# Kernel optimization log

Measured on AMD Instinct MI355X. Metric: run time of the kernel, lower is better.

The kernel has to match this reference:

```python
import math
import jax, jax.numpy as jnp
import numpy as np

B, S, D, H, L, V = 2, 1024, 1024, 16, 6, 256
HD = D // H  # 64
PAD = 0


def setup_inputs() -> dict:
    key = jax.random.key(0)
    ks = jax.random.split(key, 22)
    s = 0.02
    f32 = jnp.float32
    inp = {
        "x": jax.random.randint(ks[0], (B, S), 0, V, dtype=jnp.int32),
        "emb": (jax.random.normal(ks[1], (V, D)) * s).astype(f32),
        "Wq": (jax.random.normal(ks[2], (L, D, D)) * s).astype(f32),
        "bq": jnp.zeros((L, D), f32),
        "Wk": (jax.random.normal(ks[3], (L, D, D)) * s).astype(f32),
        "bk": jnp.zeros((L, D), f32),
        "Wv": (jax.random.normal(ks[4], (L, D, D)) * s).astype(f32),
        "bv": jnp.zeros((L, D), f32),
        "Wo": (jax.random.normal(ks[5], (L, D, D)) * s).astype(f32),
        "bo": jnp.zeros((L, D), f32),
        "W1": (jax.random.normal(ks[6], (L, D, D // 2)) * s).astype(f32),
        "b1": jnp.zeros((L, D // 2), f32),
        "W2": (jax.random.normal(ks[7], (L, D // 2, D)) * s).astype(f32),
        "b2": jnp.zeros((L, D), f32),
        "g1": jnp.ones((L, D), f32),
        "be1": jnp.zeros((L, D), f32),
        "g2": jnp.ones((L, D), f32),
        "be2": jnp.zeros((L, D), f32),
        "E": jax.random.normal(ks[8], (L, S, HD)).astype(f32),  # relative pos embeddings, non-trainable
        "Wf": (jax.random.normal(ks[9], (D, V)) * s).astype(f32),
        "bf": jnp.zeros((V,), f32),
    }
    return inp


def _layernorm(x, g, b, eps=1e-6):
    mu = jnp.mean(x, axis=-1, keepdims=True)
    var = jnp.mean((x - mu) ** 2, axis=-1, keepdims=True)
    return (x - mu) * jax.lax.rsqrt(var + eps) * g + b


def _pos_encoding():
    # embed[p, i] = sin(p * exp(-ln(1e4)*i/D) * exp(ln(1e4)*(i%2)/D) + 0.5*pi*(i%2))
    i = jnp.arange(D, dtype=jnp.float32)
    par = jnp.mod(i, 2.0)
    rate = jnp.exp(-math.log(10000.0) * i / D) * jnp.exp(math.log(10000.0) * par / D)
    pos = jnp.arange(S, dtype=jnp.float32)
    return jnp.sin(pos[:, None] * rate[None, :] + 0.5 * math.pi * par[None, :])  # [S, D]


def _skew(QE):
    # Music Transformer skewing: pad one col on the left, reshape, drop first row.
    padded = jnp.pad(QE, ((0, 0), (0, 0), (0, 0), (1, 0)))  # [B,H,S,S+1]
    reshaped = padded.reshape(B, H, S + 1, S)
    return reshaped[:, :, 1:, :]  # [B,H,S,S]


def reference(x, emb, Wq, bq, Wk, bk, Wv, bv, Wo, bo, W1, b1, W2, b2,
              g1, be1, g2, be2, E, Wf, bf):
    pe = _pos_encoding()
    # look-ahead mask: pad positions OR strictly-future positions
    pad_mask = (x == PAD)[:, None, None, :]                      # [B,1,1,S]
    causal = jnp.triu(jnp.ones((S, S), bool), k=1)[None, None]   # [1,1,S,S]
    neg = (pad_mask | causal).astype(jnp.float32) * -1e9         # [B,1,S,S]
    # QE mask: keep qe[i, j] only where j >= S-1-i (upper-right triangle)
    idx = jnp.arange(S)
    qe_mask = (idx[None, :] >= (S - 1 - idx)[:, None]).astype(jnp.float32)

    h = emb[x] * math.sqrt(D) + pe[None]  # [B,S,D]
    scale = 1.0 / math.sqrt(HD)
    for l in range(L):
        q = (h @ Wq[l] + bq[l]).reshape(B, S, H, HD).transpose(0, 2, 1, 3)
        k = (h @ Wk[l] + bk[l]).reshape(B, S, H, HD).transpose(0, 2, 1, 3)
        v = (h @ Wv[l] + bv[l]).reshape(B, S, H, HD).transpose(0, 2, 1, 3)
        QE = jnp.einsum('bhld,md->bhlm', q, E[l]) * qe_mask
        Srel = _skew(QE)
        logits = (jnp.einsum('bhld,bhmd->bhlm', q, k) + Srel) * scale + neg
        aw = jax.nn.softmax(logits, axis=-1)
        attn = jnp.einsum('bhlm,bhmd->bhld', aw, v)
        attn = attn.transpose(0, 2, 1, 3).reshape(B, S, D)
        ao = attn @ Wo[l] + bo[l]
        o1 = _layernorm(ao, g1[l], be1[l])          # NOTE: no residual, as in source
        f = jax.nn.relu(o1 @ W1[l] + b1[l]) @ W2[l] + b2[l]
        h = _layernorm(f, g2[l], be2[l])
    return h @ Wf + bf  # [B,S,V]
```

## Files before the change

### kernel.cpp

```cpp
#include <hip/hip_runtime.h>
#include <hip/hip_bf16.h>


typedef __attribute__((ext_vector_type(8))) short  s8_t;
typedef __attribute__((ext_vector_type(4))) short  s4_t;
typedef __attribute__((ext_vector_type(8))) __bf16 bf8_t;
typedef __attribute__((ext_vector_type(4))) float  f4v;

static __device__ __forceinline__ short f2bf(float f) {
  union { float f; unsigned u; } a; a.f = f;
  unsigned u = a.u;
  u += 0x7fffu + ((u >> 16) & 1u);
  return (short)(u >> 16);
}
static __device__ __forceinline__ float bf2f(short s) {
  union { float f; unsigned u; } a;
  a.u = ((unsigned)(unsigned short)s) << 16;
  return a.f;
}
static __device__ __forceinline__ f4v mfma16(s8_t a, s8_t b, f4v c) {
  return __builtin_amdgcn_mfma_f32_16x16x32_bf16(
      __builtin_bit_cast(bf8_t, a), __builtin_bit_cast(bf8_t, b), c, 0, 0, 0);
}
static __device__ __forceinline__ void gld16(const short* g, short* l) {
  __builtin_amdgcn_global_load_lds(
      (const __attribute__((address_space(1))) void*)g,
      (__attribute__((address_space(3))) void*)l, 16, 0, 0);
}

static __device__ const int IT_TAB[40] = {
  15,15,15,15, 14,14,14,14, 13,13,13,13, 12,12,12,12,
  11,11,11, 10,10,10, 9,9,9, 8,8,8,
  7,7, 6,6, 5,5, 4,4, 3, 2, 1, 0};
static __device__ const int CW_TAB[40] = {
  0,1,2,3, 0,1,2,3, 0,1,2,3, 0,1,2,3,
  0,1,2, 0,1,2, 0,1,2, 0,1,2,
  0,1, 0,1, 0,1, 0,1, 0, 0, 0, 0};

__global__ __launch_bounds__(256) void prep_weights(
    const float* __restrict__ Wq, const float* __restrict__ Wk,
    const float* __restrict__ Wv, const float* __restrict__ Wo,
    const float* __restrict__ W1, const float* __restrict__ W2,
    const float* __restrict__ Wf,
    short* __restrict__ qkvT, short* __restrict__ WoT, short* __restrict__ W1T,
    short* __restrict__ W2T, short* __restrict__ WfT) {
  __shared__ float tile[64][69];
  int z = blockIdx.x;
  const float* in; short* out; int R, C; long outBS; int rowOff = 0;
  if (z < 4608) {
    R = 1024; C = 1024; outBS = (long)3072 * 1024; out = qkvT;
    if (z < 1536)      { in = Wq; }
    else if (z < 3072) { in = Wk; rowOff = 1024; z -= 1536; }
    else               { in = Wv; rowOff = 2048; z -= 3072; }
  } else if (z < 6144) { in = Wo; out = WoT; R = 1024; C = 1024; outBS = (long)1024 * 1024; z -= 4608; }
  else if (z < 6912)   { in = W1; out = W1T; R = 1024; C = 512;  outBS = (long)512 * 1024;  z -= 6144; }
  else if (z < 7680)   { in = W2; out = W2T; R = 512;  C = 1024; outBS = (long)1024 * 512;  z -= 6912; }
  else                 { in = Wf; out = WfT; R = 1024; C = 256;  outBS = 0;                 z -= 7680; }
  const int nx = C >> 6, ny = R >> 6;
  const int per = nx * ny;
  const int l = z / per, rem = z % per;
  const int cx = rem % nx, cy = rem / nx;
  in += (long)l * R * C;
  out += (long)l * outBS + (long)rowOff * R;
  const int c0 = cx * 64, r0 = cy * 64;
  const int tid = threadIdx.x;

  const int lr = tid >> 4, lc4 = tid & 15;
#pragma unroll
  for (int p = 0; p < 4; p++) {
    const int row = p * 16 + lr;
    const float4 v = *(const float4*)(in + (long)(r0 + row) * C + c0 + lc4 * 4);
    tile[row][lc4 * 4 + 0] = v.x;
    tile[row][lc4 * 4 + 1] = v.y;
    tile[row][lc4 * 4 + 2] = v.z;
    tile[row][lc4 * 4 + 3] = v.w;
  }
  __syncthreads();
  const int seg = tid & 7;
#pragma unroll
  for (int q = 0; q < 2; q++) {
    const int oc = q * 32 + (tid >> 3);
    s8_t o;
#pragma unroll
    for (int j = 0; j < 8; j++) o[j] = f2bf(tile[seg * 8 + j][oc]);
    *(s8_t*)(out + (long)(c0 + oc) * R + r0 + seg * 8) = o;
  }
}

__global__ __launch_bounds__(256) void prep_misc(
    const int* __restrict__ x, const float* __restrict__ emb,
    const float* __restrict__ E,
    const float* __restrict__ bq, const float* __restrict__ bk,
    const float* __restrict__ bv,
    short* __restrict__ h, short* __restrict__ Ebf,
    float* __restrict__ qkvB, int* __restrict__ fnp) {
  const int z = blockIdx.x;
  const int tid = threadIdx.x;
  if (z < 2048) {
    const int s = z & 1023;
    const int xv = x[z];
    const int c = tid << 2;
    const float4 e = *(const float4*)(emb + (long)xv * 1024 + c);
    const float ev[4] = {e.x, e.y, e.z, e.w};
    s4_t o;
#pragma unroll
    for (int i = 0; i < 4; i++) {
      const int d = c + i;
      const float par = (float)(d & 1);
      const float rate = expf(-9.210340371976184f * (float)d / 1024.0f) *
                         expf(9.210340371976184f * par / 1024.0f);
      const float pe = sinf((float)s * rate + 1.5707963267948966f * par);
      o[i] = f2bf(ev[i] * 32.0f + pe);
    }
    *(s4_t*)(h + (long)z * 1024 + c) = o;
  } else if (z < 2432) {
    const long i = ((long)(z - 2048) * 256 + tid) * 4;
    const float4 t = *(const float4*)(E + i);
    s4_t o = {f2bf(t.x), f2bf(t.y), f2bf(t.z), f2bf(t.w)};
    *(s4_t*)(Ebf + i) = o;
  } else if (z < 2504) {
    const int idx = (z - 2432) * 256 + tid;
    const int l = idx / 3072, n = idx % 3072;
    float v = (n < 1024) ? bq[l * 1024 + n]
            : (n < 2048) ? bk[l * 1024 + n - 1024]
                         : bv[l * 1024 + n - 2048];
    qkvB[idx] = v;
  } else {
    if (tid < 64) {
      const int b = z - 2504;
      int first = 1024;
      for (int j0 = 0; j0 < 1024; j0 += 64) {
        unsigned long long m = __ballot(x[b * 1024 + j0 + tid] != 0);
        if (m) { first = j0 + __ffsll(m) - 1; break; }
      }
      if (tid == 0) fnp[b] = first;
    }
  }
}

__global__ __launch_bounds__(256) void ln_kernel(const short* __restrict__ in,
                                                 short* __restrict__ out,
                                                 const float* __restrict__ g,
                                                 const float* __restrict__ be) {
  __shared__ float red[4];
  __shared__ float red2[4];
  const int row = blockIdx.x;
  const int tid = threadIdx.x;
  const int c = tid << 2;
  const s4_t xv = *(const s4_t*)(in + (long)row * 1024 + c);
  const float x0 = bf2f(xv[0]), x1 = bf2f(xv[1]), x2 = bf2f(xv[2]), x3 = bf2f(xv[3]);
  float s = x0 + x1 + x2 + x3;
#pragma unroll
  for (int off = 1; off < 64; off <<= 1) s += __shfl_xor(s, off);
  const int wave = tid >> 6, lane = tid & 63;
  if (lane == 0) red[wave] = s;
  __syncthreads();
  const float mu = (red[0] + red[1] + red[2] + red[3]) * (1.0f / 1024.0f);
  const float d0 = x0 - mu, d1 = x1 - mu, d2 = x2 - mu, d3 = x3 - mu;
  float q = d0 * d0 + d1 * d1 + d2 * d2 + d3 * d3;
#pragma unroll
  for (int off = 1; off < 64; off <<= 1) q += __shfl_xor(q, off);
  if (lane == 0) red2[wave] = q;
  __syncthreads();
  const float var = (red2[0] + red2[1] + red2[2] + red2[3]) * (1.0f / 1024.0f);
  const float rs = rsqrtf(var + 1e-6f);
  const float4 gv = *(const float4*)(g + c);
  const float4 bv = *(const float4*)(be + c);
  s4_t o = {f2bf(d0 * rs * gv.x + bv.x), f2bf(d1 * rs * gv.y + bv.y),
            f2bf(d2 * rs * gv.z + bv.z), f2bf(d3 * rs * gv.w + bv.w)};
  *(s4_t*)(out + (long)row * 1024 + c) = o;
}

template <int BM, int BN, int WR, int WC, int OUT_BF16, int RELU>
__global__ __launch_bounds__(256) void gemm_lds(
    const short* __restrict__ A, const short* __restrict__ BT,
    void* __restrict__ Cv, const float* __restrict__ biasp,
    int K, int lda, int ldb, int ldc) {
  constexpr int AR = BM / 64, BR = BN / 64;
  constexpr int FI = BM / WR / 16, FJ = BN / WC / 16;
  __shared__ short As[BM * 32];
  __shared__ short Bs[BN * 32];
  const int bm = blockIdx.y * BM, bn = blockIdx.x * BN;
  const int tid = threadIdx.x;
  const int wave = tid >> 6, lane = tid & 63;
  const int quad = lane >> 4, l16 = lane & 15;
  const int wr = wave / WC, wc = wave % WC;
  const int wm = wr * (BM / WR), wn = wc * (BN / WC);

  const short* Ag = A + (long)(bm + wave * 16 + (lane >> 2)) * lda + ((lane & 3) << 3);
  const short* Bg = BT + (long)(bn + wave * 16 + (lane >> 2)) * ldb + ((lane & 3) << 3);

  f4v acc[FI][FJ];
#pragma unroll
  for (int i = 0; i < FI; i++)
#pragma unroll
    for (int j = 0; j < FJ; j++) {
      f4v zz = {0.f, 0.f, 0.f, 0.f};
      acc[i][j] = zz;
    }

  for (int k0 = 0; k0 < K; k0 += 32) {
#pragma unroll
    for (int r = 0; r < AR; r++)
      gld16(Ag + (long)r * 64 * lda + k0, As + r * 2048 + wave * 512);
#pragma unroll
    for (int r = 0; r < BR; r++)
      gld16(Bg + (long)r * 64 * ldb + k0, Bs + r * 2048 + wave * 512);
    __syncthreads();
    s8_t af[FI], bfr[FJ];
#pragma unroll
    for (int t = 0; t < FI; t++)
      af[t] = *(const s8_t*)&As[(wm + t * 16 + l16) * 32 + quad * 8];
#pragma unroll
    for (int t = 0; t < FJ; t++)
      bfr[t] = *(const s8_t*)&Bs[(wn + t * 16 + l16) * 32 + quad * 8];
#pragma unroll
    for (int ti = 0; ti < FI; ti++)
#pragma unroll
      for (int tj = 0; tj < FJ; tj++)
        acc[ti][tj] = mfma16(af[ti], bfr[tj], acc[ti][tj]);
    __syncthreads();
  }

#pragma unroll
  for (int ti = 0; ti < FI; ti++) {
#pragma unroll
    for (int tj = 0; tj < FJ; tj++) {
      const int n = bn + wn + tj * 16 + l16;
      const float bval = biasp ? biasp[n] : 0.f;
#pragma unroll
      for (int r = 0; r < 4; r++) {
        const int m = bm + wm + ti * 16 + quad * 4 + r;
        float vv = acc[ti][tj][r] + bval;
        if (RELU) vv = fmaxf(vv, 0.f);
        if (OUT_BF16) ((short*)Cv)[(long)m * ldc + n] = f2bf(vv);
        else          ((float*)Cv)[(long)m * ldc + n] = vv;
      }
    }
  }
}

__global__ __launch_bounds__(256) void attn_main(
    const short* __restrict__ qkv, const short* __restrict__ Eb,
    const int* __restrict__ xids, const int* __restrict__ fnp,
    float* __restrict__ PO, float* __restrict__ PM, float* __restrict__ PL,
    short* __restrict__ outb) {
  __shared__ short Ks2[2][8][64][8];
  __shared__ short Vt[64][72];
  __shared__ short Gs[4][16][88];
  __shared__ short knegs[1024];

  const int bh = blockIdx.x, b = bh >> 4, hh = bh & 15;
  const int yy = blockIdx.y;
  const bool fbp = (yy >= 40);
  const int itile = fbp ? (yy - 40) : IT_TAB[yy];
  const int cw = fbp ? 0 : CW_TAB[yy];
  const int fb = fnp[b];
  const int i0g = itile * 64;
  if (fbp && fb <= i0g) return;

  const int tid = threadIdx.x;
  const int wave = tid >> 6, lane = tid & 63, quad = lane >> 4, l16 = lane & 15;
  const int i0 = i0g + wave * 16;

  {
    const short neg = f2bf(-1e9f);
#pragma unroll
    for (int t = 0; t < 4; t++) {
      const int idx = t * 256 + tid;
      knegs[idx] = (xids[b * 1024 + idx] == 0) ? neg : (short)0;
    }
  }

  s8_t aq[2];
  {
    const short* qp = qkv + ((long)(b * 1024 + i0 + l16)) * 3072 + hh * 64 + quad * 8;
    aq[0] = *(const s8_t*)qp;
    aq[1] = *(const s8_t*)(qp + 32);
  }

  f4v o[4];
#pragma unroll
  for (int nt = 0; nt < 4; nt++) { f4v zz = {0.f, 0.f, 0.f, 0.f}; o[nt] = zz; }
  float m_run[4] = {-INFINITY, -INFINITY, -INFINITY, -INFINITY};
  float l_run[4] = {0.f, 0.f, 0.f, 0.f};

  const short* kbase = qkv + (long)b * 1024 * 3072 + 1024 + hh * 64 + wave * 8;
  const short* vbase = qkv + (long)b * 1024 * 3072 + 2048 + hh * 64 + wave * 16;
  short* gs = &Gs[wave][0][0];

  const int jBeg = fbp ? 0 : cw * 256;
  const int jEnd = fbp ? 1024 : min(cw * 256 + 256, i0g + 64);

  s8_t vr0, vr1;
  {
    const long k1 = min(jBeg + lane, 1023);
    gld16(kbase + k1 * 3072, &Ks2[0][wave][0][0]);
    gld16(kbase + k1 * 3072 + 32, &Ks2[0][wave + 4][0][0]);
    const short* vrow = vbase + k1 * 3072;
    vr0 = *(const s8_t*)(vrow);
    vr1 = *(const s8_t*)(vrow + 8);
#pragma unroll
    for (int t = 0; t < 8; t++) {
      Vt[wave * 16 + t][lane] = vr0[t];
      Vt[wave * 16 + 8 + t][lane] = vr1[t];
    }
  }

  int pb = 0;
  for (int j0 = jBeg; j0 < jEnd; j0 += 64) {
    const bool hasNext = (j0 + 64 < jEnd);
    __syncthreads();

    {
      const int mW = 1008 - i0g - wave * 16 + j0;
#pragma unroll
      for (int t = 0; t < 5; t++) {
        const int m = min(mW + t * 16 + l16, 1023);
        const short* ep = Eb + m * 64 + quad * 8;
        const s8_t eb0 = *(const s8_t*)ep;
        const s8_t eb1 = *(const s8_t*)(ep + 32);
        f4v g = {0.f, 0.f, 0.f, 0.f};
        g = mfma16(aq[0], eb0, g);
        g = mfma16(aq[1], eb1, g);
#pragma unroll
        for (int r = 0; r < 4; r++)
          gs[(quad * 4 + r) * 88 + t * 16 + l16] = f2bf(g[r]);
      }
    }

    if (hasNext) {
      const long k1 = min(j0 + 64 + lane, 1023);
      gld16(kbase + k1 * 3072, &Ks2[pb ^ 1][wave][0][0]);
      gld16(kbase + k1 * 3072 + 32, &Ks2[pb ^ 1][wave + 4][0][0]);
      const short* vrow = vbase + k1 * 3072;
      vr0 = *(const s8_t*)(vrow);
      vr1 = *(const s8_t*)(vrow + 8);
    }

    float p[4][4];
    const int irow = i0 + quad * 4;
#pragma unroll
    for (int jt = 0; jt < 4; jt++) {
      const s8_t k0f = *(const s8_t*)&Ks2[pb][quad][jt * 16 + l16][0];
      const s8_t k1f = *(const s8_t*)&Ks2[pb][4 + quad][jt * 16 + l16][0];
      f4v zz = {0.f, 0.f, 0.f, 0.f};
      zz = mfma16(aq[0], k0f, zz);
      zz = mfma16(aq[1], k1f, zz);
      const int j = j0 + jt * 16 + l16;
      const float kn = bf2f(knegs[j]);
#pragma unroll
      for (int r = 0; r < 4; r++) {
        const int rr = quad * 4 + r;
        const float smv = bf2f(gs[rr * 87 + 15 + jt * 16 + l16]);
        const bool causal = (j <= irow + r);
        const float srel = causal ? smv : 0.f;
        const float kk = fbp ? 0.f : (causal ? kn : -1e9f);
        p[jt][r] = (zz[r] + srel) * 0.125f + kk;
      }
    }

    float alpha[4];
#pragma unroll
    for (int r = 0; r < 4; r++) {
      float mx = p[0][r];
#pragma unroll
      for (int jt = 1; jt < 4; jt++) mx = fmaxf(mx, p[jt][r]);
      mx = fmaxf(mx, __shfl_xor(mx, 1));
      mx = fmaxf(mx, __shfl_xor(mx, 2));
      mx = fmaxf(mx, __shfl_xor(mx, 4));
      mx = fmaxf(mx, __shfl_xor(mx, 8));
      const float mnew = fmaxf(m_run[r], mx);
      alpha[r] = __expf(m_run[r] - mnew);
      float ps = 0.f;
#pragma unroll
      for (int jt = 0; jt < 4; jt++) {
        p[jt][r] = __expf(p[jt][r] - mnew);
        ps += p[jt][r];
      }
      ps += __shfl_xor(ps, 1);
      ps += __shfl_xor(ps, 2);
      ps += __shfl_xor(ps, 4);
      ps += __shfl_xor(ps, 8);
      l_run[r] = l_run[r] * alpha[r] + ps;
      m_run[r] = mnew;
    }

#pragma unroll
    for (int jt = 0; jt < 4; jt++)
#pragma unroll
      for (int r = 0; r < 4; r++)
        gs[(quad * 4 + r) * 88 + jt * 16 + l16] = f2bf(p[jt][r]);
#pragma unroll
    for (int nt = 0; nt < 4; nt++)
#pragma unroll
      for (int r = 0; r < 4; r++)
        o[nt][r] *= alpha[r];

#pragma unroll
    for (int ks4 = 0; ks4 < 2; ks4++) {
      const s8_t ap = *(const s8_t*)&gs[l16 * 88 + ks4 * 32 + quad * 8];
#pragma unroll
      for (int nt = 0; nt < 4; nt++) {
        const s8_t vf = *(const s8_t*)&Vt[nt * 16 + l16][ks4 * 32 + quad * 8];
        o[nt] = mfma16(ap, vf, o[nt]);
      }
    }

    __syncthreads();
    if (hasNext) {
#pragma unroll
      for (int t = 0; t < 8; t++) {
        Vt[wave * 16 + t][lane] = vr0[t];
        Vt[wave * 16 + 8 + t][lane] = vr1[t];
      }
    }
    pb ^= 1;
  }

  if (fbp) {
#pragma unroll
    for (int nt = 0; nt < 4; nt++)
#pragma unroll
      for (int r = 0; r < 4; r++) {
        const int i = i0 + quad * 4 + r;
        if (i < fb)
          outb[((long)(b * 1024 + i)) * 1024 + hh * 64 + nt * 16 + l16] =
              f2bf(o[nt][r] / l_run[r]);
      }
  } else if (yy >= 36) {
#pragma unroll
    for (int nt = 0; nt < 4; nt++)
#pragma unroll
      for (int r = 0; r < 4; r++) {
        const int i = i0 + quad * 4 + r;
        if (i >= fb)
          outb[((long)(b * 1024 + i)) * 1024 + hh * 64 + nt * 16 + l16] =
              f2bf(o[nt][r] / l_run[r]);
      }
  } else {
    const long part = (long)(bh * 16 + itile) * 4 + cw;
    float* po = PO + part * 4096;
#pragma unroll
    for (int nt = 0; nt < 4; nt++)
#pragma unroll
      for (int r = 0; r < 4; r++) {
        const int row = wave * 16 + quad * 4 + r;
        po[row * 64 + nt * 16 + l16] = o[nt][r];
      }
    if (l16 == 0) {
#pragma unroll
      for (int r = 0; r < 4; r++) {
        const int row = wave * 16 + quad * 4 + r;
        PM[part * 64 + row] = m_run[r];
        PL[part * 64 + row] = l_run[r];
      }
    }
  }
}

__global__ __launch_bounds__(256) void attn_combine(
    const float* __restrict__ PO, const float* __restrict__ PM,
    const float* __restrict__ PL, const int* __restrict__ fnp,
    short* __restrict__ outb) {
  const int id = blockIdx.x;
  const int bh = id / 12, itile = 4 + id % 12;
  const int b = bh >> 4, hh = bh & 15;
  const int nc = (itile >> 2) + 1;
  const int row = threadIdx.x >> 2, seg = (threadIdx.x & 3) << 4;
  const long base = (long)(bh * 16 + itile) * 4;
  const int i = itile * 64 + row;
  if (i < fnp[b]) return;

  float mv[4];
  float M = -INFINITY;
  for (int c = 0; c < nc; c++) {
    mv[c] = PM[(base + c) * 64 + row];
    M = fmaxf(M, mv[c]);
  }
  f4v acc[4];
#pragma unroll
  for (int t = 0; t < 4; t++) { f4v zz = {0.f, 0.f, 0.f, 0.f}; acc[t] = zz; }
  float l = 0.f;
  for (int c = 0; c < nc; c++) {
    const float w = __expf(mv[c] - M);
    l += w * PL[(base + c) * 64 + row];
    const float* po = PO + (base + c) * 4096 + row * 64 + seg;
#pragma unroll
    for (int t = 0; t < 4; t++) {
      const f4v v = *(const f4v*)(po + t * 4);
      acc[t] += w * v;
    }
  }
  const float inv = 1.0f / l;
  short* op = outb + ((long)(b * 1024 + i)) * 1024 + hh * 64 + seg;
#pragma unroll
  for (int t = 0; t < 4; t++) {
    s4_t o = {f2bf(acc[t][0] * inv), f2bf(acc[t][1] * inv),
              f2bf(acc[t][2] * inv), f2bf(acc[t][3] * inv)};
    *(s4_t*)(op + t * 4) = o;
  }
}

extern "C" void kernel_launch(void* const* d_in, const int* in_sizes, int n_in,
                              void* d_out, int out_size, void* d_ws, size_t ws_size,
                              hipStream_t stream) {
  const int*   x   = (const int*)d_in[0];
  const float* emb = (const float*)d_in[1];
  const float* Wq  = (const float*)d_in[2];
  const float* bq  = (const float*)d_in[3];
  const float* Wk  = (const float*)d_in[4];
  const float* bk  = (const float*)d_in[5];
  const float* Wv  = (const float*)d_in[6];
  const float* bv  = (const float*)d_in[7];
  const float* Wo  = (const float*)d_in[8];
  const float* bo  = (const float*)d_in[9];
  const float* W1  = (const float*)d_in[10];
  const float* b1  = (const float*)d_in[11];
  const float* W2  = (const float*)d_in[12];
  const float* b2  = (const float*)d_in[13];
  const float* g1  = (const float*)d_in[14];
  const float* be1 = (const float*)d_in[15];
  const float* g2  = (const float*)d_in[16];
  const float* be2 = (const float*)d_in[17];
  const float* E   = (const float*)d_in[18];
  const float* Wf  = (const float*)d_in[19];
  const float* bfv = (const float*)d_in[20];

  char* p = (char*)d_ws;
  auto alloc = [&](size_t bytes) {
    char* r = p;
    p += (bytes + 255) & ~(size_t)255;
    return r;
  };
  short* h    = (short*)alloc(2048ull * 1024 * 2);
  short* qkv  = (short*)alloc(2048ull * 3072 * 2);
  short* attn = (short*)alloc(2048ull * 1024 * 2);
  short* tmp  = (short*)alloc(2048ull * 1024 * 2);
  short* mid  = (short*)alloc(2048ull * 512 * 2);
  short* qkvT = (short*)alloc(6ull * 3072 * 1024 * 2);
  short* WoT  = (short*)alloc(6ull * 1024 * 1024 * 2);
  short* W1T  = (short*)alloc(6ull * 512 * 1024 * 2);
  short* W2T  = (short*)alloc(6ull * 1024 * 512 * 2);
  short* WfT  = (short*)alloc(256ull * 1024 * 2);
  short* Ebf  = (short*)alloc(6ull * 1024 * 64 * 2);
  float* qkvB = (float*)alloc(6ull * 3072 * 4);
  int*   fnp  = (int*)alloc(256);
  float* PO   = (float*)alloc(2048ull * 4096 * 4);
  float* PM   = (float*)alloc(2048ull * 64 * 4);
  float* PL   = (float*)alloc(2048ull * 64 * 4);

  prep_weights<<<7744, 256, 0, stream>>>(
      Wq, Wk, Wv, Wo, W1, W2, Wf, qkvT, WoT, W1T, W2T, WfT);
  prep_misc<<<2506, 256, 0, stream>>>(x, emb, E, bq, bk, bv, h, Ebf, qkvB, fnp);

  for (int l = 0; l < 6; l++) {
    const long wOff = (long)l * 1024 * 1024;
    const long w12Off = (long)l * 512 * 1024;
    gemm_lds<128, 128, 2, 2, 1, 0><<<dim3(24, 16), 256, 0, stream>>>(
        h, qkvT + (long)l * 3072 * 1024, qkv, qkvB + l * 3072, 1024, 1024, 1024, 3072);
    attn_main<<<dim3(32, 56), 256, 0, stream>>>(
        qkv, Ebf + (long)l * 1024 * 64, x, fnp, PO, PM, PL, attn);
    attn_combine<<<384, 256, 0, stream>>>(PO, PM, PL, fnp, attn);
    gemm_lds<64, 64, 2, 2, 1, 0><<<dim3(16, 32), 256, 0, stream>>>(
        attn, WoT + wOff, tmp, bo + l * 1024, 1024, 1024, 1024, 1024);
    ln_kernel<<<2048, 256, 0, stream>>>(tmp, tmp, g1 + l * 1024, be1 + l * 1024);
    gemm_lds<64, 64, 2, 2, 1, 1><<<dim3(8, 32), 256, 0, stream>>>(
        tmp, W1T + w12Off, mid, b1 + l * 512, 1024, 1024, 1024, 512);
    gemm_lds<64, 64, 2, 2, 1, 0><<<dim3(16, 32), 256, 0, stream>>>(
        mid, W2T + w12Off, h, b2 + l * 1024, 512, 512, 512, 1024);
    ln_kernel<<<2048, 256, 0, stream>>>(h, h, g2 + l * 1024, be2 + l * 1024);
  }
  gemm_lds<64, 64, 2, 2, 0, 0><<<dim3(4, 32), 256, 0, stream>>>(
      h, WfT, (float*)d_out, bfv, 1024, 1024, 1024, 256);
}
```

Before: 973.5 us.

## Process 128 query rows per attention block to share K/V tiles

Each attention block now handles two 64-row query groups against the same staged K/V tiles, which halves K/V global and LDS traffic per query row. The grid shrinks from 56 to 28 y-blocks, with new tile and chunk tables for 128-row tiles. The partial-output buffers and the combine kernel are re-indexed to match. In exchange, register pressure rises from two accumulator sets, there are fewer blocks, and some fully masked causal work is done on diagonal tiles.

```diff
diff --git a/kernel.cpp b/kernel.cpp
--- a/kernel.cpp
+++ b/kernel.cpp
@@ -28,14 +28,10 @@
       (__attribute__((address_space(3))) void*)l, 16, 0, 0);
 }
 
-static __device__ const int IT_TAB[40] = {
-  15,15,15,15, 14,14,14,14, 13,13,13,13, 12,12,12,12,
-  11,11,11, 10,10,10, 9,9,9, 8,8,8,
-  7,7, 6,6, 5,5, 4,4, 3, 2, 1, 0};
-static __device__ const int CW_TAB[40] = {
-  0,1,2,3, 0,1,2,3, 0,1,2,3, 0,1,2,3,
-  0,1,2, 0,1,2, 0,1,2, 0,1,2,
-  0,1, 0,1, 0,1, 0,1, 0, 0, 0, 0};
+static __device__ const int IT_TAB[20] = {
+  7,7,7,7, 6,6,6, 5,5,5, 4,4, 3,3, 2, 1, 6, 4, 2, 0};
+static __device__ const int CW_TAB[20] = {
+  0,1,2,3, 0,1,2, 0,1,2, 0,1, 0,1, 0, 0, 3, 2, 1, 0};
 
 __global__ __launch_bounds__(256) void prep_weights(
     const float* __restrict__ Wq, const float* __restrict__ Wk,
@@ -252,16 +248,15 @@
 
   const int bh = blockIdx.x, b = bh >> 4, hh = bh & 15;
   const int yy = blockIdx.y;
-  const bool fbp = (yy >= 40);
-  const int itile = fbp ? (yy - 40) : IT_TAB[yy];
+  const bool fbp = (yy >= 20);
+  const int itile = fbp ? (yy - 20) : IT_TAB[yy];
   const int cw = fbp ? 0 : CW_TAB[yy];
   const int fb = fnp[b];
-  const int i0g = itile * 64;
+  const int i0g = itile * 128;
   if (fbp && fb <= i0g) return;
 
   const int tid = threadIdx.x;
   const int wave = tid >> 6, lane = tid & 63, quad = lane >> 4, l16 = lane & 15;
-  const int i0 = i0g + wave * 16;
 
   {
     const short neg = f2bf(-1e9f);
@@ -272,25 +267,38 @@
     }
   }
 
-  s8_t aq[2];
+  const int i0A = i0g + wave * 16;
+  const int i0B = i0g + 64 + wave * 16;
+
+  s8_t aqA[2], aqB[2];
   {
-    const short* qp = qkv + ((long)(b * 1024 + i0 + l16)) * 3072 + hh * 64 + quad * 8;
-    aq[0] = *(const s8_t*)qp;
-    aq[1] = *(const s8_t*)(qp + 32);
-  }
-
-  f4v o[4];
-#pragma unroll
-  for (int nt = 0; nt < 4; nt++) { f4v zz = {0.f, 0.f, 0.f, 0.f}; o[nt] = zz; }
-  float m_run[4] = {-INFINITY, -INFINITY, -INFINITY, -INFINITY};
-  float l_run[4] = {0.f, 0.f, 0.f, 0.f};
+    const short* qp = qkv + ((long)(b * 1024 + i0A + l16)) * 3072 + hh * 64 + quad * 8;
+    aqA[0] = *(const s8_t*)qp;
+    aqA[1] = *(const s8_t*)(qp + 32);
+    const short* qp2 = qp + 64 * 3072;
+    aqB[0] = *(const s8_t*)qp2;
+    aqB[1] = *(const s8_t*)(qp2 + 32);
+  }
+
+  f4v oA[4], oB[4];
+#pragma unroll
+  for (int nt = 0; nt < 4; nt++) {
+    f4v zz = {0.f, 0.f, 0.f, 0.f};
+    oA[nt] = zz; oB[nt] = zz;
+  }
+  float mA[4], lA[4], mB[4], lB[4];
+#pragma unroll
+  for (int r = 0; r < 4; r++) {
+    mA[r] = -INFINITY; mB[r] = -INFINITY;
+    lA[r] = 0.f; lB[r] = 0.f;
+  }
 
   const short* kbase = qkv + (long)b * 1024 * 3072 + 1024 + hh * 64 + wave * 8;
   const short* vbase = qkv + (long)b * 1024 * 3072 + 2048 + hh * 64 + wave * 16;
   short* gs = &Gs[wave][0][0];
 
   const int jBeg = fbp ? 0 : cw * 256;
-  const int jEnd = fbp ? 1024 : min(cw * 256 + 256, i0g + 64);
+  const int jEnd = fbp ? 1024 : min(cw * 256 + 256, i0g + 128);
 
   s8_t vr0, vr1;
   {
@@ -307,13 +315,10 @@
     }
   }
 
-  int pb = 0;
-  for (int j0 = jBeg; j0 < jEnd; j0 += 64) {
-    const bool hasNext = (j0 + 64 < jEnd);
-    __syncthreads();
-
+  auto pass = [&](const s8_t* aq, f4v* o, float* m_run, float* l_run,
+                  const int i0, const int pb, const int j0) {
     {
-      const int mW = 1008 - i0g - wave * 16 + j0;
+      const int mW = 1008 - i0 + j0;
 #pragma unroll
       for (int t = 0; t < 5; t++) {
         const int m = min(mW + t * 16 + l16, 1023);
@@ -329,15 +334,6 @@
       }
     }
 
-    if (hasNext) {
-      const long k1 = min(j0 + 64 + lane, 1023);
-      gld16(kbase + k1 * 3072, &Ks2[pb ^ 1][wave][0][0]);
-      gld16(kbase + k1 * 3072 + 32, &Ks2[pb ^ 1][wave + 4][0][0]);
-      const short* vrow = vbase + k1 * 3072;
-      vr0 = *(const s8_t*)(vrow);
-      vr1 = *(const s8_t*)(vrow + 8);
-    }
-
     float p[4][4];
     const int irow = i0 + quad * 4;
 #pragma unroll
@@ -406,6 +402,24 @@
         o[nt] = mfma16(ap, vf, o[nt]);
       }
     }
+  };
+
+  int pb = 0;
+  for (int j0 = jBeg; j0 < jEnd; j0 += 64) {
+    const bool hasNext = (j0 + 64 < jEnd);
+    __syncthreads();
+
+    if (hasNext) {
+      const long k1 = min(j0 + 64 + lane, 1023);
+      gld16(kbase + k1 * 3072, &Ks2[pb ^ 1][wave][0][0]);
+      gld16(kbase + k1 * 3072 + 32, &Ks2[pb ^ 1][wave + 4][0][0]);
+      const short* vrow = vbase + k1 * 3072;
+      vr0 = *(const s8_t*)(vrow);
+      vr1 = *(const s8_t*)(vrow + 8);
+    }
+
+    pass(aqA, oA, mA, lA, i0A, pb, j0);
+    pass(aqB, oB, mB, lB, i0B, pb, j0);
 
     __syncthreads();
     if (hasNext) {
@@ -423,37 +437,50 @@
     for (int nt = 0; nt < 4; nt++)
 #pragma unroll
       for (int r = 0; r < 4; r++) {
-        const int i = i0 + quad * 4 + r;
-        if (i < fb)
-          outb[((long)(b * 1024 + i)) * 1024 + hh * 64 + nt * 16 + l16] =
-              f2bf(o[nt][r] / l_run[r]);
-      }
-  } else if (yy >= 36) {
+        const int iA = i0A + quad * 4 + r;
+        if (iA < fb)
+          outb[((long)(b * 1024 + iA)) * 1024 + hh * 64 + nt * 16 + l16] =
+              f2bf(oA[nt][r] / lA[r]);
+        const int iB = i0B + quad * 4 + r;
+        if (iB < fb)
+          outb[((long)(b * 1024 + iB)) * 1024 + hh * 64 + nt * 16 + l16] =
+              f2bf(oB[nt][r] / lB[r]);
+      }
+  } else if (itile <= 1) {
 #pragma unroll
     for (int nt = 0; nt < 4; nt++)
 #pragma unroll
       for (int r = 0; r < 4; r++) {
-        const int i = i0 + quad * 4 + r;
-        if (i >= fb)
-          outb[((long)(b * 1024 + i)) * 1024 + hh * 64 + nt * 16 + l16] =
-              f2bf(o[nt][r] / l_run[r]);
+        const int iA = i0A + quad * 4 + r;
+        if (iA >= fb)
+          outb[((long)(b * 1024 + iA)) * 1024 + hh * 64 + nt * 16 + l16] =
+              f2bf(oA[nt][r] / lA[r]);
+        const int iB = i0B + quad * 4 + r;
+        if (iB >= fb)
+          outb[((long)(b * 1024 + iB)) * 1024 + hh * 64 + nt * 16 + l16] =
+              f2bf(oB[nt][r] / lB[r]);
       }
   } else {
-    const long part = (long)(bh * 16 + itile) * 4 + cw;
-    float* po = PO + part * 4096;
+    const long part = (long)(bh * 8 + itile) * 4 + cw;
+    float* po = PO + part * 8192;
 #pragma unroll
     for (int nt = 0; nt < 4; nt++)
 #pragma unroll
       for (int r = 0; r < 4; r++) {
-        const int row = wave * 16 + quad * 4 + r;
-        po[row * 64 + nt * 16 + l16] = o[nt][r];
+        const int rowA = wave * 16 + quad * 4 + r;
+        po[rowA * 64 + nt * 16 + l16] = oA[nt][r];
+        const int rowB = 64 + wave * 16 + quad * 4 + r;
+        po[rowB * 64 + nt * 16 + l16] = oB[nt][r];
       }
     if (l16 == 0) {
 #pragma unroll
       for (int r = 0; r < 4; r++) {
-        const int row = wave * 16 + quad * 4 + r;
-        PM[part * 64 + row] = m_run[r];
-        PL[part * 64 + row] = l_run[r];
+        const int rowA = wave * 16 + quad * 4 + r;
+        PM[part * 128 + rowA] = mA[r];
+        PL[part * 128 + rowA] = lA[r];
+        const int rowB = 64 + wave * 16 + quad * 4 + r;
+        PM[part * 128 + rowB] = mB[r];
+        PL[part * 128 + rowB] = lB[r];
       }
     }
   }
@@ -464,18 +491,20 @@
     const float* __restrict__ PL, const int* __restrict__ fnp,
     short* __restrict__ outb) {
   const int id = blockIdx.x;
-  const int bh = id / 12, itile = 4 + id % 12;
+  const int bh = id / 12, rem = id % 12;
+  const int itile = 2 + (rem >> 1), half = rem & 1;
   const int b = bh >> 4, hh = bh & 15;
-  const int nc = (itile >> 2) + 1;
+  const int nc = (itile >> 1) + 1;
   const int row = threadIdx.x >> 2, seg = (threadIdx.x & 3) << 4;
-  const long base = (long)(bh * 16 + itile) * 4;
-  const int i = itile * 64 + row;
+  const int prow = half * 64 + row;
+  const long base = (long)(bh * 8 + itile) * 4;
+  const int i = itile * 128 + prow;
   if (i < fnp[b]) return;
 
   float mv[4];
   float M = -INFINITY;
   for (int c = 0; c < nc; c++) {
-    mv[c] = PM[(base + c) * 64 + row];
+    mv[c] = PM[(base + c) * 128 + prow];
     M = fmaxf(M, mv[c]);
   }
   f4v acc[4];
@@ -484,8 +513,8 @@
   float l = 0.f;
   for (int c = 0; c < nc; c++) {
     const float w = __expf(mv[c] - M);
-    l += w * PL[(base + c) * 64 + row];
-    const float* po = PO + (base + c) * 4096 + row * 64 + seg;
+    l += w * PL[(base + c) * 128 + prow];
+    const float* po = PO + (base + c) * 8192 + prow * 64 + seg;
 #pragma unroll
     for (int t = 0; t < 4; t++) {
       const f4v v = *(const f4v*)(po + t * 4);
@@ -546,9 +575,9 @@
   short* Ebf  = (short*)alloc(6ull * 1024 * 64 * 2);
   float* qkvB = (float*)alloc(6ull * 3072 * 4);
   int*   fnp  = (int*)alloc(256);
-  float* PO   = (float*)alloc(2048ull * 4096 * 4);
-  float* PM   = (float*)alloc(2048ull * 64 * 4);
-  float* PL   = (float*)alloc(2048ull * 64 * 4);
+  float* PO   = (float*)alloc(1024ull * 8192 * 4);
+  float* PM   = (float*)alloc(1024ull * 128 * 4);
+  float* PL   = (float*)alloc(1024ull * 128 * 4);
 
   prep_weights<<<7744, 256, 0, stream>>>(
       Wq, Wk, Wv, Wo, W1, W2, Wf, qkvT, WoT, W1T, W2T, WfT);
@@ -559,7 +588,7 @@
     const long w12Off = (long)l * 512 * 1024;
     gemm_lds<128, 128, 2, 2, 1, 0><<<dim3(24, 16), 256, 0, stream>>>(
         h, qkvT + (long)l * 3072 * 1024, qkv, qkvB + l * 3072, 1024, 1024, 1024, 3072);
-    attn_main<<<dim3(32, 56), 256, 0, stream>>>(
+    attn_main<<<dim3(32, 28), 256, 0, stream>>>(
         qkv, Ebf + (long)l * 1024 * 64, x, fnp, PO, PM, PL, attn);
     attn_combine<<<384, 256, 0, stream>>>(PO, PM, PL, fnp, attn);
     gemm_lds<64, 64, 2, 2, 1, 0><<<dim3(16, 32), 256, 0, stream>>>(
```

Result: slower. 997.9 us (+2.5%).
